# Kernel optimization log

Hardware: AMD Instinct MI355X
Metric: run time of the kernel (lower is better)

The kernel has to match this reference:

```python
import jax, jax.numpy as jnp
import numpy as np

B, D_IN, D_OUT, N_SUBNET, G = 16384, 512, 512, 8, 2


def setup_inputs() -> dict:
    key = jax.random.key(0)
    k_x, k_g, k_w = jax.random.split(key, 3)
    x = jax.random.normal(k_x, (B, D_IN), dtype=jnp.float32)
    groups = jax.random.randint(k_g, (B, G), 0, N_SUBNET, dtype=jnp.int32)
    # per-expert Dense params (the 'subnets')
    W = jax.random.normal(k_w, (N_SUBNET, D_IN, D_OUT), dtype=jnp.float32) * (1.0 / np.sqrt(D_IN))
    b = jnp.zeros((N_SUBNET, D_OUT), dtype=jnp.float32)
    return {"x": x, "groups": groups, "W": W, "b": b}


def reference(x, groups, W, b):
    """SubnetGate: one-hot gated dispatch to per-group subnets + combine.

    Faithful math: gates = one_hot(groups[:, group_col], n_subnet);
    out = sum_e gates[:, e] * subnet_e(x). Since gates are one-hot the
    combine selects exactly one expert output per row (gate weight 1.0).
    """
    group_col = 0
    n_subnet = W.shape[0]
    idx_group = groups[:, group_col]                     # [B]
    gates = jax.nn.one_hot(idx_group, n_subnet, dtype=x.dtype)  # [B, E]
    # run every expert on the full batch (dense reference for the
    # gather-compute-scatter kernel), then gate-combine
    expert_out = jnp.einsum("bi,eio->beo", x, W) + b[None, :, :]  # [B, E, O]
    out = jnp.einsum("be,beo->bo", gates, expert_out)             # [B, O]
    return out
```

## Files before the change

### kernel.cpp

```cpp
#include <hip/hip_runtime.h>
#include <hip/hip_bf16.h>


#define NROWS   16384
#define KDIM    512
#define NDIM    512
#define NEXP    8
#define BM      128
#define BN      128
#define BK      64
#define NT_PER  4
#define KT_PER  8
#define TILE_ELEMS (BN * BK)
#define WS_ROWLIST_OFF 4096
#define WS_WT_OFF      (4096 + NEXP * NROWS * 4)
#define WS_XG_OFF      (WS_WT_OFF + (size_t)NEXP * NT_PER * KT_PER * TILE_ELEMS * 2)
#define WS_NEEDED      (WS_XG_OFF + (size_t)NROWS * KDIM * 2)

typedef __bf16        bf16x8 __attribute__((ext_vector_type(8)));
typedef float         f32x4  __attribute__((ext_vector_type(4)));
typedef unsigned int  u32x4  __attribute__((ext_vector_type(4)));

__device__ __forceinline__ unsigned int f2bf_u(float f) {
    unsigned int u = __builtin_bit_cast(unsigned int, f);
    return (u + 0x7FFFu + ((u >> 16) & 1u)) >> 16;
}

__device__ __forceinline__ void gl_lds16(const void* g, void* l) {
    __builtin_amdgcn_global_load_lds(
        (const __attribute__((address_space(1))) unsigned int*)g,
        (__attribute__((address_space(3))) unsigned int*)l, 16, 0, 0);
}

__device__ __forceinline__ bf16x8 pack_bf8(f32x4 lo, f32x4 hi) {
    u32x4 w;
    w.x = f2bf_u(lo.x) | (f2bf_u(lo.y) << 16);
    w.y = f2bf_u(lo.z) | (f2bf_u(lo.w) << 16);
    w.z = f2bf_u(hi.x) | (f2bf_u(hi.y) << 16);
    w.w = f2bf_u(hi.z) | (f2bf_u(hi.w) << 16);
    return __builtin_bit_cast(bf16x8, w);
}

__global__ void prep_kernel(const float* __restrict__ W,
                            const float* __restrict__ x,
                            const int* __restrict__ groups,
                            int* __restrict__ counts,
                            int* __restrict__ rowlist,
                            unsigned short* __restrict__ Wtile,
                            unsigned short* __restrict__ xg) {
    const int bid = blockIdx.x;
    const int tid = threadIdx.x;

    if (bid < 8) {
        __shared__ int wcnt_s[4];
        __shared__ int woff_s[4];
        __shared__ int runb;
        const int e  = bid;
        const int w  = tid >> 6;
        const int ln = tid & 63;
        const unsigned long long below = (ln == 63) ? ~0ull >> 1
                                                    : (1ull << ln) - 1;
        int* dst = rowlist + e * NROWS;
        if (tid == 0) runb = 0;
        __syncthreads();
        for (int it = 0; it < NROWS / 2048; ++it) {
            int rbase = it * 2048 + tid * 8;
            u32x4 g0 = *(const u32x4*)&groups[rbase * 2];
            u32x4 g1 = *(const u32x4*)&groups[rbase * 2 + 4];
            u32x4 g2 = *(const u32x4*)&groups[rbase * 2 + 8];
            u32x4 g3 = *(const u32x4*)&groups[rbase * 2 + 12];
            bool h[8] = {(int)g0.x == e, (int)g0.z == e,
                         (int)g1.x == e, (int)g1.z == e,
                         (int)g2.x == e, (int)g2.z == e,
                         (int)g3.x == e, (int)g3.z == e};
            unsigned long long m[8];
            int c[8], tot = 0;
            #pragma unroll
            for (int jj = 0; jj < 8; ++jj) {
                m[jj] = __ballot(h[jj]);
                c[jj] = __popcll(m[jj]);
                tot += c[jj];
            }
            if (ln == 0) wcnt_s[w] = tot;
            __syncthreads();
            if (tid == 0) {
                int s = runb;
                #pragma unroll
                for (int i = 0; i < 4; ++i) { woff_s[i] = s; s += wcnt_s[i]; }
                runb = s;
            }
            __syncthreads();
            int base = woff_s[w];
            #pragma unroll
            for (int jj = 0; jj < 8; ++jj) {
                if (h[jj]) dst[base + __popcll(m[jj] & below)] = rbase + jj;
                base += c[jj];
            }
            __syncthreads();
        }
        if (tid == 0) counts[e] = runb;
    } else if (bid < 1032) {
        __shared__ __align__(16) unsigned short tl4[32 * 64];
        const int tb   = bid - 8;
        const int tile = tb >> 2;
        const int qq   = tb & 3;
        const int e  = tile >> 5;
        const int nt = (tile >> 3) & 3;
        const int kt = tile & 7;
        const float* Wb = W + (size_t)e * (KDIM * NDIM);

        const int n   = qq * 32 + (tid & 31);
        const int g   = tid >> 5;
        const int col = nt * BN + n;
        unsigned int p[4];
        #pragma unroll
        for (int jj = 0; jj < 4; ++jj) {
            int k0 = kt * BK + g * 8 + jj * 2;
            unsigned int lo = f2bf_u(Wb[(size_t)k0 * NDIM + col]);
            unsigned int hi = f2bf_u(Wb[(size_t)(k0 + 1) * NDIM + col]);
            p[jj] = lo | (hi << 16);
        }
        *(u32x4*)&tl4[(n & 31) * 64 + (g ^ (n & 7)) * 8] = *(const u32x4*)p;
        __syncthreads();
        unsigned short* dst = Wtile + (size_t)tile * TILE_ELEMS
                                    + ((size_t)qq * 256 + tid) * 8;
        *(u32x4*)dst = *(const u32x4*)&tl4[tid * 8];
    } else {
        const size_t base = ((size_t)(bid - 1032) * 256 + tid) * 16;
        f32x4 v0 = *(const f32x4*)&x[base];
        f32x4 v1 = *(const f32x4*)&x[base + 4];
        f32x4 v2 = *(const f32x4*)&x[base + 8];
        f32x4 v3 = *(const f32x4*)&x[base + 12];
        *(bf16x8*)&xg[base]     = pack_bf8(v0, v1);
        *(bf16x8*)&xg[base + 8] = pack_bf8(v2, v3);
    }
}


#define STAGE_B(KT, BUF)                                                     \
    {                                                                        \
        const unsigned short* _src = wt + (size_t)(KT) * TILE_ELEMS;         \
        _Pragma("unroll")                                                    \
        for (int _i = 0; _i < 4; ++_i) {                                     \
            int _off = (_i * 256 + tid) * 8;                                 \
            gl_lds16(_src + _off, &Bsm[BUF][_off]);                          \
        }                                                                    \
    }

#define LOAD_A_XG(KT, AR)                                                    \
    {                                                                        \
        const unsigned short* _p0 = arow0 + (KT) * BK + q * 8;               \
        const unsigned short* _p1 = arow1 + (KT) * BK + q * 8;               \
        AR[0][0] = *(const bf16x8*)_p0;                                      \
        AR[0][1] = *(const bf16x8*)(_p0 + 32);                               \
        AR[1][0] = *(const bf16x8*)_p1;                                      \
        AR[1][1] = *(const bf16x8*)(_p1 + 32);                               \
    }

#define LOAD_A_F32(KT, AR)                                                   \
    {                                                                        \
        const float* _p0 = afrow0 + (KT) * BK + q * 8;                       \
        const float* _p1 = afrow1 + (KT) * BK + q * 8;                       \
        AR[0][0] = pack_bf8(*(const f32x4*)_p0, *(const f32x4*)(_p0 + 4));   \
        AR[0][1] = pack_bf8(*(const f32x4*)(_p0 + 32),                       \
                            *(const f32x4*)(_p0 + 36));                      \
        AR[1][0] = pack_bf8(*(const f32x4*)_p1, *(const f32x4*)(_p1 + 4));   \
        AR[1][1] = pack_bf8(*(const f32x4*)(_p1 + 32),                       \
                            *(const f32x4*)(_p1 + 36));                      \
    }

#define COMPUTE(BUF, AR)                                                     \
    {                                                                        \
        _Pragma("unroll")                                                    \
        for (int _h = 0; _h < 2; ++_h) {                                     \
            _Pragma("unroll")                                                \
            for (int _ni = 0; _ni < 8; ++_ni) {                              \
                int _n = _ni * 16 + l15;                                     \
                bf16x8 _bf = *(const bf16x8*)&Bsm[BUF][_n * 64 +             \
                             ((_h * 4 + q) ^ (_n & 7)) * 8];                 \
                acc[0][_ni] = __builtin_amdgcn_mfma_f32_16x16x32_bf16(       \
                    AR[0][_h], _bf, acc[0][_ni], 0, 0, 0);                   \
                acc[1][_ni] = __builtin_amdgcn_mfma_f32_16x16x32_bf16(       \
                    AR[1][_h], _bf, acc[1][_ni], 0, 0, 0);                   \
            }                                                                \
        }                                                                    \
    }

#define KSTEP(KT, VM, ACUR, ANXT, LOADA)                                     \
    {                                                                        \
        asm volatile("s_waitcnt vmcnt(" #VM ")" ::: "memory");               \
        __builtin_amdgcn_s_barrier();                                        \
        __builtin_amdgcn_sched_barrier(0);                                   \
        if ((KT) + 2 < KT_PER) LOADA((KT) + 2, ANXT)                         \
        if ((KT) + 3 < KT_PER) STAGE_B((KT) + 3, ((KT) + 3) & 3)             \
        __builtin_amdgcn_s_setprio(1);                                       \
        COMPUTE((KT) & 3, ACUR)                                              \
        __builtin_amdgcn_s_setprio(0);                                       \
    }

#define KLOOP(LOADA)                                                         \
    {                                                                        \
        LOADA(0, aA)                                                         \
        LOADA(1, aB)                                                         \
        KSTEP(0, 16, aA, aC, LOADA)                                          \
        KSTEP(1, 20, aB, aA, LOADA)                                          \
        KSTEP(2, 24, aC, aB, LOADA)                                          \
        KSTEP(3, 16, aA, aC, LOADA)                                          \
        KSTEP(4, 16, aB, aA, LOADA)                                          \
        KSTEP(5, 16, aC, aB, LOADA)                                          \
        KSTEP(6, 12, aA, aC, LOADA)                                          \
        KSTEP(7, 4,  aB, aA, LOADA)                                          \
    }

__global__ __launch_bounds__(256, 2)
void gemm_kernel(const float* __restrict__ x,
                 const unsigned short* __restrict__ xg,
                 const int* __restrict__ counts,
                 const int* __restrict__ rowlist,
                 const unsigned short* __restrict__ Wtile,
                 const float* __restrict__ bias,
                 float* __restrict__ out) {
    __shared__ __align__(16) unsigned short Bsm[4][TILE_ELEMS];

    const int bid = blockIdx.x;
    const int e   = bid & 7;
    const int j   = bid >> 3;
    const int nt  = j & 3;
    const int mt  = j >> 2;
    const int cnt = counts[e];
    const int rb  = mt * BM;
    if (rb >= cnt) return;
    int m_valid = cnt - rb;
    if (m_valid > BM) m_valid = BM;
    const int* rl = rowlist + e * NROWS + rb;

    const int tid = threadIdx.x;
    const int w   = tid >> 6;
    const int ln  = tid & 63;
    const int q   = ln >> 4;
    const int l15 = ln & 15;
    const int wm  = w * 32;

    const int r0i = wm + l15;
    const int r1i = wm + 16 + l15;
    const int ri0 = (r0i < m_valid) ? r0i : 0;
    const int ri1 = (r1i < m_valid) ? r1i : 0;

    const unsigned short* wt =
        Wtile + (size_t)((e * NT_PER + nt) * KT_PER) * TILE_ELEMS;

    f32x4 acc[2][8];
    #pragma unroll
    for (int mi = 0; mi < 2; ++mi)
        #pragma unroll
        for (int ni = 0; ni < 8; ++ni)
            acc[mi][ni] = (f32x4){0.f, 0.f, 0.f, 0.f};

    bf16x8 aA[2][2], aB[2][2], aC[2][2];

    STAGE_B(0, 0)
    STAGE_B(1, 1)
    STAGE_B(2, 2)

    if (xg != nullptr) {
        const unsigned short* arow0 = xg + (size_t)rl[ri0] * KDIM;
        const unsigned short* arow1 = xg + (size_t)rl[ri1] * KDIM;
        KLOOP(LOAD_A_XG)
    } else {
        const float* afrow0 = x + (size_t)rl[ri0] * KDIM;
        const float* afrow1 = x + (size_t)rl[ri1] * KDIM;
        KLOOP(LOAD_A_F32)
    }

    int grow[2][4];
    #pragma unroll
    for (int mi = 0; mi < 2; ++mi)
        #pragma unroll
        for (int r = 0; r < 4; ++r) {
            int mloc = wm + mi * 16 + q * 4 + r;
            grow[mi][r] = (mloc < m_valid) ? rl[mloc] : -1;
        }
    const int ncol0 = nt * BN;
    #pragma unroll
    for (int ni = 0; ni < 8; ++ni) {
        int col = ncol0 + ni * 16 + l15;
        float bv = bias[e * NDIM + col];
        #pragma unroll
        for (int mi = 0; mi < 2; ++mi)
            #pragma unroll
            for (int r = 0; r < 4; ++r)
                if (grow[mi][r] >= 0)
                    __builtin_nontemporal_store(acc[mi][ni][r] + bv,
                        &out[(size_t)grow[mi][r] * NDIM + col]);
    }
}

extern "C" void kernel_launch(void* const* d_in, const int* in_sizes, int n_in,
                              void* d_out, int out_size, void* d_ws, size_t ws_size,
                              hipStream_t stream) {
    const float* x      = (const float*)d_in[0];
    const int*   groups = (const int*)d_in[1];
    const float* W      = (const float*)d_in[2];
    const float* b      = (const float*)d_in[3];
    float*       out    = (float*)d_out;

    char* ws = (char*)d_ws;
    int*            counts  = (int*)ws;
    int*            rowlist = (int*)(ws + WS_ROWLIST_OFF);
    unsigned short* Wtile   = (unsigned short*)(ws + WS_WT_OFF);
    const bool use_xg = (ws_size >= WS_NEEDED);
    unsigned short* xg = use_xg ? (unsigned short*)(ws + WS_XG_OFF) : nullptr;

    prep_kernel<<<use_xg ? 3080 : 1032, 256, 0, stream>>>(
        W, x, groups, counts, rowlist, Wtile, xg);
    gemm_kernel<<<4096, 256, 0, stream>>>(x, xg, counts, rowlist, Wtile, b, out);
}
```

Before: 128.7 us.

## Switch GEMM to full-width 64-row tiles with 512-thread blocks and BK=32

Each block now computes a 64x512 output tile for one expert with 8 waves, instead of 128x128 tiles with 4 waves. Full output width is covered per block, so each gathered A row is loaded once per expert tile rather than once per N-tile. The weight pre-transform now writes 32x512 k-slices without swizzling. B is staged through 128KB of dynamic LDS, which is likely to allow only one block per CU. Each B fragment read from LDS now feeds one MFMA instead of two, and the unswizzled LDS layout may cause bank conflicts.

```diff
diff --git a/kernel.cpp b/kernel.cpp
--- a/kernel.cpp
+++ b/kernel.cpp
@@ -6,15 +6,13 @@
 #define KDIM    512
 #define NDIM    512
 #define NEXP    8
-#define BM      128
-#define BN      128
-#define BK      64
-#define NT_PER  4
-#define KT_PER  8
-#define TILE_ELEMS (BN * BK)
+#define BM      64
+#define BK      32
+#define KT_PER  16
+#define TILE_SH 16384
 #define WS_ROWLIST_OFF 4096
 #define WS_WT_OFF      (4096 + NEXP * NROWS * 4)
-#define WS_XG_OFF      (WS_WT_OFF + (size_t)NEXP * NT_PER * KT_PER * TILE_ELEMS * 2)
+#define WS_XG_OFF      (WS_WT_OFF + (size_t)NEXP * KT_PER * TILE_SH * 2)
 #define WS_NEEDED      (WS_XG_OFF + (size_t)NROWS * KDIM * 2)
 
 typedef __bf16        bf16x8 __attribute__((ext_vector_type(8)));
@@ -99,34 +97,35 @@
             __syncthreads();
         }
         if (tid == 0) counts[e] = runb;
-    } else if (bid < 1032) {
-        __shared__ __align__(16) unsigned short tl4[32 * 64];
-        const int tb   = bid - 8;
-        const int tile = tb >> 2;
-        const int qq   = tb & 3;
-        const int e  = tile >> 5;
-        const int nt = (tile >> 3) & 3;
-        const int kt = tile & 7;
+    } else if (bid < 136) {
+        __shared__ __align__(16) unsigned short tl[TILE_SH];
+        const int t  = bid - 8;
+        const int e  = t >> 4;
+        const int kt = t & 15;
         const float* Wb = W + (size_t)e * (KDIM * NDIM);
-
-        const int n   = qq * 32 + (tid & 31);
-        const int g   = tid >> 5;
-        const int col = nt * BN + n;
-        unsigned int p[4];
         #pragma unroll
-        for (int jj = 0; jj < 4; ++jj) {
-            int k0 = kt * BK + g * 8 + jj * 2;
-            unsigned int lo = f2bf_u(Wb[(size_t)k0 * NDIM + col]);
-            unsigned int hi = f2bf_u(Wb[(size_t)(k0 + 1) * NDIM + col]);
-            p[jj] = lo | (hi << 16);
+        for (int it = 0; it < 8; ++it) {
+            const int n = (it & 1) * 256 + tid;
+            const int g = it >> 1;
+            const int k0 = kt * BK + g * 8;
+            unsigned int p[4];
+            #pragma unroll
+            for (int jj = 0; jj < 4; ++jj) {
+                unsigned int lo = f2bf_u(Wb[(size_t)(k0 + jj * 2) * NDIM + n]);
+                unsigned int hi = f2bf_u(Wb[(size_t)(k0 + jj * 2 + 1) * NDIM + n]);
+                p[jj] = lo | (hi << 16);
+            }
+            *(u32x4*)&tl[n * 32 + g * 8] = *(const u32x4*)p;
         }
-        *(u32x4*)&tl4[(n & 31) * 64 + (g ^ (n & 7)) * 8] = *(const u32x4*)p;
         __syncthreads();
-        unsigned short* dst = Wtile + (size_t)tile * TILE_ELEMS
-                                    + ((size_t)qq * 256 + tid) * 8;
-        *(u32x4*)dst = *(const u32x4*)&tl4[tid * 8];
+        unsigned short* dst = Wtile + (size_t)t * TILE_SH;
+        #pragma unroll
+        for (int it = 0; it < 8; ++it) {
+            int off = (it * 256 + tid) * 8;
+            *(u32x4*)&dst[off] = *(const u32x4*)&tl[off];
+        }
     } else {
-        const size_t base = ((size_t)(bid - 1032) * 256 + tid) * 16;
+        const size_t base = ((size_t)(bid - 136) * 256 + tid) * 16;
         f32x4 v0 = *(const f32x4*)&x[base];
         f32x4 v1 = *(const f32x4*)&x[base + 4];
         f32x4 v2 = *(const f32x4*)&x[base + 8];
@@ -137,52 +136,36 @@
 }
 
 
+extern __shared__ __align__(16) unsigned short Bsm[];
+
 #define STAGE_B(KT, BUF)                                                     \
     {                                                                        \
-        const unsigned short* _src = wt + (size_t)(KT) * TILE_ELEMS;         \
+        const unsigned short* _src = wt + (size_t)(KT) * TILE_SH;            \
         _Pragma("unroll")                                                    \
         for (int _i = 0; _i < 4; ++_i) {                                     \
-            int _off = (_i * 256 + tid) * 8;                                 \
-            gl_lds16(_src + _off, &Bsm[BUF][_off]);                          \
+            int _off = (_i * 512 + tid) * 8;                                 \
+            gl_lds16(_src + _off, &Bsm[(BUF) * TILE_SH + _off]);             \
         }                                                                    \
     }
 
 #define LOAD_A_XG(KT, AR)                                                    \
-    {                                                                        \
-        const unsigned short* _p0 = arow0 + (KT) * BK + q * 8;               \
-        const unsigned short* _p1 = arow1 + (KT) * BK + q * 8;               \
-        AR[0][0] = *(const bf16x8*)_p0;                                      \
-        AR[0][1] = *(const bf16x8*)(_p0 + 32);                               \
-        AR[1][0] = *(const bf16x8*)_p1;                                      \
-        AR[1][1] = *(const bf16x8*)(_p1 + 32);                               \
-    }
+    { AR = *(const bf16x8*)(arow + (KT) * BK + q * 8); }
 
 #define LOAD_A_F32(KT, AR)                                                   \
     {                                                                        \
-        const float* _p0 = afrow0 + (KT) * BK + q * 8;                       \
-        const float* _p1 = afrow1 + (KT) * BK + q * 8;                       \
-        AR[0][0] = pack_bf8(*(const f32x4*)_p0, *(const f32x4*)(_p0 + 4));   \
-        AR[0][1] = pack_bf8(*(const f32x4*)(_p0 + 32),                       \
-                            *(const f32x4*)(_p0 + 36));                      \
-        AR[1][0] = pack_bf8(*(const f32x4*)_p1, *(const f32x4*)(_p1 + 4));   \
-        AR[1][1] = pack_bf8(*(const f32x4*)(_p1 + 32),                       \
-                            *(const f32x4*)(_p1 + 36));                      \
+        const float* _p = afrow + (KT) * BK + q * 8;                         \
+        AR = pack_bf8(*(const f32x4*)_p, *(const f32x4*)(_p + 4));           \
     }
 
 #define COMPUTE(BUF, AR)                                                     \
     {                                                                        \
         _Pragma("unroll")                                                    \
-        for (int _h = 0; _h < 2; ++_h) {                                     \
-            _Pragma("unroll")                                                \
-            for (int _ni = 0; _ni < 8; ++_ni) {                              \
-                int _n = _ni * 16 + l15;                                     \
-                bf16x8 _bf = *(const bf16x8*)&Bsm[BUF][_n * 64 +             \
-                             ((_h * 4 + q) ^ (_n & 7)) * 8];                 \
-                acc[0][_ni] = __builtin_amdgcn_mfma_f32_16x16x32_bf16(       \
-                    AR[0][_h], _bf, acc[0][_ni], 0, 0, 0);                   \
-                acc[1][_ni] = __builtin_amdgcn_mfma_f32_16x16x32_bf16(       \
-                    AR[1][_h], _bf, acc[1][_ni], 0, 0, 0);                   \
-            }                                                                \
+        for (int _ni = 0; _ni < 16; ++_ni) {                                 \
+            int _nn = nh + _ni * 16 + l15;                                   \
+            bf16x8 _bf = *(const bf16x8*)&Bsm[(BUF) * TILE_SH +              \
+                                              _nn * 32 + q * 8];             \
+            acc[_ni] = __builtin_amdgcn_mfma_f32_16x16x32_bf16(              \
+                AR, _bf, acc[_ni], 0, 0, 0);                                 \
         }                                                                    \
     }
 
@@ -202,17 +185,25 @@
     {                                                                        \
         LOADA(0, aA)                                                         \
         LOADA(1, aB)                                                         \
-        KSTEP(0, 16, aA, aC, LOADA)                                          \
-        KSTEP(1, 20, aB, aA, LOADA)                                          \
-        KSTEP(2, 24, aC, aB, LOADA)                                          \
-        KSTEP(3, 16, aA, aC, LOADA)                                          \
-        KSTEP(4, 16, aB, aA, LOADA)                                          \
-        KSTEP(5, 16, aC, aB, LOADA)                                          \
-        KSTEP(6, 12, aA, aC, LOADA)                                          \
-        KSTEP(7, 4,  aB, aA, LOADA)                                          \
-    }
-
-__global__ __launch_bounds__(256, 2)
+        KSTEP(0,  10, aA, aC, LOADA)                                         \
+        KSTEP(1,  11, aB, aA, LOADA)                                         \
+        KSTEP(2,  12, aC, aB, LOADA)                                         \
+        KSTEP(3,  10, aA, aC, LOADA)                                         \
+        KSTEP(4,  10, aB, aA, LOADA)                                         \
+        KSTEP(5,  10, aC, aB, LOADA)                                         \
+        KSTEP(6,  10, aA, aC, LOADA)                                         \
+        KSTEP(7,  10, aB, aA, LOADA)                                         \
+        KSTEP(8,  10, aC, aB, LOADA)                                         \
+        KSTEP(9,  10, aA, aC, LOADA)                                         \
+        KSTEP(10, 10, aB, aA, LOADA)                                         \
+        KSTEP(11, 10, aC, aB, LOADA)                                         \
+        KSTEP(12, 10, aA, aC, LOADA)                                         \
+        KSTEP(13, 10, aB, aA, LOADA)                                         \
+        KSTEP(14, 6,  aC, aB, LOADA)                                         \
+        KSTEP(15, 1,  aA, aC, LOADA)                                         \
+    }
+
+__global__ __launch_bounds__(512, 2)
 void gemm_kernel(const float* __restrict__ x,
                  const unsigned short* __restrict__ xg,
                  const int* __restrict__ counts,
@@ -220,13 +211,9 @@
                  const unsigned short* __restrict__ Wtile,
                  const float* __restrict__ bias,
                  float* __restrict__ out) {
-    __shared__ __align__(16) unsigned short Bsm[4][TILE_ELEMS];
-
     const int bid = blockIdx.x;
     const int e   = bid & 7;
-    const int j   = bid >> 3;
-    const int nt  = j & 3;
-    const int mt  = j >> 2;
+    const int mt  = bid >> 3;
     const int cnt = counts[e];
     const int rb  = mt * BM;
     if (rb >= cnt) return;
@@ -239,59 +226,47 @@
     const int ln  = tid & 63;
     const int q   = ln >> 4;
     const int l15 = ln & 15;
-    const int wm  = w * 32;
-
-    const int r0i = wm + l15;
-    const int r1i = wm + 16 + l15;
-    const int ri0 = (r0i < m_valid) ? r0i : 0;
-    const int ri1 = (r1i < m_valid) ? r1i : 0;
-
-    const unsigned short* wt =
-        Wtile + (size_t)((e * NT_PER + nt) * KT_PER) * TILE_ELEMS;
-
-    f32x4 acc[2][8];
+    const int s   = w >> 1;
+    const int nh  = (w & 1) * 256;
+
+    const int am = s * 16 + l15;
+    const int ri = (am < m_valid) ? am : 0;
+
+    const unsigned short* wt = Wtile + (size_t)e * KT_PER * TILE_SH;
+
+    f32x4 acc[16];
     #pragma unroll
-    for (int mi = 0; mi < 2; ++mi)
-        #pragma unroll
-        for (int ni = 0; ni < 8; ++ni)
-            acc[mi][ni] = (f32x4){0.f, 0.f, 0.f, 0.f};
-
-    bf16x8 aA[2][2], aB[2][2], aC[2][2];
+    for (int ni = 0; ni < 16; ++ni) acc[ni] = (f32x4){0.f, 0.f, 0.f, 0.f};
+
+    bf16x8 aA, aB, aC;
 
     STAGE_B(0, 0)
     STAGE_B(1, 1)
     STAGE_B(2, 2)
 
     if (xg != nullptr) {
-        const unsigned short* arow0 = xg + (size_t)rl[ri0] * KDIM;
-        const unsigned short* arow1 = xg + (size_t)rl[ri1] * KDIM;
+        const unsigned short* arow = xg + (size_t)rl[ri] * KDIM;
         KLOOP(LOAD_A_XG)
     } else {
-        const float* afrow0 = x + (size_t)rl[ri0] * KDIM;
-        const float* afrow1 = x + (size_t)rl[ri1] * KDIM;
+        const float* afrow = x + (size_t)rl[ri] * KDIM;
         KLOOP(LOAD_A_F32)
     }
 
-    int grow[2][4];
+    int grow[4];
     #pragma unroll
-    for (int mi = 0; mi < 2; ++mi)
-        #pragma unroll
-        for (int r = 0; r < 4; ++r) {
-            int mloc = wm + mi * 16 + q * 4 + r;
-            grow[mi][r] = (mloc < m_valid) ? rl[mloc] : -1;
-        }
-    const int ncol0 = nt * BN;
+    for (int r = 0; r < 4; ++r) {
+        int mloc = s * 16 + q * 4 + r;
+        grow[r] = (mloc < m_valid) ? rl[mloc] : -1;
+    }
     #pragma unroll
-    for (int ni = 0; ni < 8; ++ni) {
-        int col = ncol0 + ni * 16 + l15;
+    for (int ni = 0; ni < 16; ++ni) {
+        int col = nh + ni * 16 + l15;
         float bv = bias[e * NDIM + col];
         #pragma unroll
-        for (int mi = 0; mi < 2; ++mi)
-            #pragma unroll
-            for (int r = 0; r < 4; ++r)
-                if (grow[mi][r] >= 0)
-                    __builtin_nontemporal_store(acc[mi][ni][r] + bv,
-                        &out[(size_t)grow[mi][r] * NDIM + col]);
+        for (int r = 0; r < 4; ++r)
+            if (grow[r] >= 0)
+                __builtin_nontemporal_store(acc[ni][r] + bv,
+                    &out[(size_t)grow[r] * NDIM + col]);
     }
 }
 
@@ -311,7 +286,16 @@
     const bool use_xg = (ws_size >= WS_NEEDED);
     unsigned short* xg = use_xg ? (unsigned short*)(ws + WS_XG_OFF) : nullptr;
 
-    prep_kernel<<<use_xg ? 3080 : 1032, 256, 0, stream>>>(
+    static bool attr_set = false;
+    if (!attr_set) {
+        hipFuncSetAttribute((const void*)gemm_kernel,
+                            hipFuncAttributeMaxDynamicSharedMemorySize,
+                            4 * TILE_SH * 2);
+        attr_set = true;
+    }
+
+    prep_kernel<<<use_xg ? 2184 : 136, 256, 0, stream>>>(
         W, x, groups, counts, rowlist, Wtile, xg);
-    gemm_kernel<<<4096, 256, 0, stream>>>(x, xg, counts, rowlist, Wtile, b, out);
-}
+    gemm_kernel<<<2048, 512, 4 * TILE_SH * 2, stream>>>(
+        x, xg, counts, rowlist, Wtile, b, out);
+}
```

Result: slower. 137.0 us (+6.4%).

## Stage whole expert weight slab in LDS once per block with 256-row tiles

Applied to the files above, without the earlier changes.

Each GEMM block now loads the full 512x128 bf16 weight slab for its expert and column strip into dynamic shared memory (128KB) up front, then runs 512 threads over a 256-row tile. It replaces the per-k-step pipelined B staging and barriers with one wait, and uses a fixed grid of 9 row chunks per expert and strip. The intent is to cut redundant weight reloads and barrier overhead. The cost is one block per CU with large LDS use, plus a grid that assumes no expert holds more than 2304 rows. Output stores also change from nontemporal to normal stores.

```diff
diff --git a/kernel.cpp b/kernel.cpp
--- a/kernel.cpp
+++ b/kernel.cpp
@@ -6,12 +6,12 @@
 #define KDIM    512
 #define NDIM    512
 #define NEXP    8
-#define BM      128
+#define BM      256
 #define BN      128
-#define BK      64
 #define NT_PER  4
 #define KT_PER  8
-#define TILE_ELEMS (BN * BK)
+#define MC_PER  9
+#define TILE_ELEMS (BN * 64)
 #define WS_ROWLIST_OFF 4096
 #define WS_WT_OFF      (4096 + NEXP * NROWS * 4)
 #define WS_XG_OFF      (WS_WT_OFF + (size_t)NEXP * NT_PER * KT_PER * TILE_ELEMS * 2)
@@ -115,7 +115,7 @@
         unsigned int p[4];
         #pragma unroll
         for (int jj = 0; jj < 4; ++jj) {
-            int k0 = kt * BK + g * 8 + jj * 2;
+            int k0 = kt * 64 + g * 8 + jj * 2;
             unsigned int lo = f2bf_u(Wb[(size_t)k0 * NDIM + col]);
             unsigned int hi = f2bf_u(Wb[(size_t)(k0 + 1) * NDIM + col]);
             p[jj] = lo | (hi << 16);
@@ -137,82 +137,62 @@
 }
 
 
-#define STAGE_B(KT, BUF)                                                     \
-    {                                                                        \
-        const unsigned short* _src = wt + (size_t)(KT) * TILE_ELEMS;         \
-        _Pragma("unroll")                                                    \
-        for (int _i = 0; _i < 4; ++_i) {                                     \
-            int _off = (_i * 256 + tid) * 8;                                 \
-            gl_lds16(_src + _off, &Bsm[BUF][_off]);                          \
-        }                                                                    \
-    }
-
-#define LOAD_A_XG(KT, AR)                                                    \
-    {                                                                        \
-        const unsigned short* _p0 = arow0 + (KT) * BK + q * 8;               \
-        const unsigned short* _p1 = arow1 + (KT) * BK + q * 8;               \
-        AR[0][0] = *(const bf16x8*)_p0;                                      \
-        AR[0][1] = *(const bf16x8*)(_p0 + 32);                               \
-        AR[1][0] = *(const bf16x8*)_p1;                                      \
-        AR[1][1] = *(const bf16x8*)(_p1 + 32);                               \
-    }
-
-#define LOAD_A_F32(KT, AR)                                                   \
-    {                                                                        \
-        const float* _p0 = afrow0 + (KT) * BK + q * 8;                       \
-        const float* _p1 = afrow1 + (KT) * BK + q * 8;                       \
-        AR[0][0] = pack_bf8(*(const f32x4*)_p0, *(const f32x4*)(_p0 + 4));   \
-        AR[0][1] = pack_bf8(*(const f32x4*)(_p0 + 32),                       \
-                            *(const f32x4*)(_p0 + 36));                      \
-        AR[1][0] = pack_bf8(*(const f32x4*)_p1, *(const f32x4*)(_p1 + 4));   \
-        AR[1][1] = pack_bf8(*(const f32x4*)(_p1 + 32),                       \
-                            *(const f32x4*)(_p1 + 36));                      \
-    }
-
-#define COMPUTE(BUF, AR)                                                     \
+extern __shared__ __align__(16) unsigned short Bsm[];
+
+#define LOAD_A_XG(QT, AR)                                                    \
     {                                                                        \
         _Pragma("unroll")                                                    \
-        for (int _h = 0; _h < 2; ++_h) {                                     \
+        for (int _kh = 0; _kh < 4; ++_kh) {                                  \
+            int _k0 = (QT) * 128 + _kh * 32 + q * 8;                         \
+            AR[0][_kh] = *(const bf16x8*)(arow0 + _k0);                      \
+            AR[1][_kh] = *(const bf16x8*)(arow1 + _k0);                      \
+        }                                                                    \
+    }
+
+#define LOAD_A_F32(QT, AR)                                                   \
+    {                                                                        \
+        _Pragma("unroll")                                                    \
+        for (int _kh = 0; _kh < 4; ++_kh) {                                  \
+            int _k0 = (QT) * 128 + _kh * 32 + q * 8;                         \
+            const float* _p0 = afrow0 + _k0;                                 \
+            const float* _p1 = afrow1 + _k0;                                 \
+            AR[0][_kh] = pack_bf8(*(const f32x4*)_p0, *(const f32x4*)(_p0 + 4)); \
+            AR[1][_kh] = pack_bf8(*(const f32x4*)_p1, *(const f32x4*)(_p1 + 4)); \
+        }                                                                    \
+    }
+
+#define COMPUTE_Q(QT, AR)                                                    \
+    {                                                                        \
+        _Pragma("unroll")                                                    \
+        for (int _kh = 0; _kh < 4; ++_kh) {                                  \
+            const int _t  = (QT) * 4 + _kh;                                  \
+            const int _kt = _t >> 1;                                         \
+            const int _g  = (_t & 1) * 4 + q;                                \
             _Pragma("unroll")                                                \
             for (int _ni = 0; _ni < 8; ++_ni) {                              \
                 int _n = _ni * 16 + l15;                                     \
-                bf16x8 _bf = *(const bf16x8*)&Bsm[BUF][_n * 64 +             \
-                             ((_h * 4 + q) ^ (_n & 7)) * 8];                 \
+                bf16x8 _bf = *(const bf16x8*)&Bsm[_kt * TILE_ELEMS +         \
+                             _n * 64 + (_g ^ (_n & 7)) * 8];                 \
                 acc[0][_ni] = __builtin_amdgcn_mfma_f32_16x16x32_bf16(       \
-                    AR[0][_h], _bf, acc[0][_ni], 0, 0, 0);                   \
+                    AR[0][_kh], _bf, acc[0][_ni], 0, 0, 0);                  \
                 acc[1][_ni] = __builtin_amdgcn_mfma_f32_16x16x32_bf16(       \
-                    AR[1][_h], _bf, acc[1][_ni], 0, 0, 0);                   \
+                    AR[1][_kh], _bf, acc[1][_ni], 0, 0, 0);                  \
             }                                                                \
         }                                                                    \
     }
 
-#define KSTEP(KT, VM, ACUR, ANXT, LOADA)                                     \
-    {                                                                        \
-        asm volatile("s_waitcnt vmcnt(" #VM ")" ::: "memory");               \
-        __builtin_amdgcn_s_barrier();                                        \
-        __builtin_amdgcn_sched_barrier(0);                                   \
-        if ((KT) + 2 < KT_PER) LOADA((KT) + 2, ANXT)                         \
-        if ((KT) + 3 < KT_PER) STAGE_B((KT) + 3, ((KT) + 3) & 3)             \
-        __builtin_amdgcn_s_setprio(1);                                       \
-        COMPUTE((KT) & 3, ACUR)                                              \
-        __builtin_amdgcn_s_setprio(0);                                       \
-    }
-
 #define KLOOP(LOADA)                                                         \
     {                                                                        \
-        LOADA(0, aA)                                                         \
-        LOADA(1, aB)                                                         \
-        KSTEP(0, 16, aA, aC, LOADA)                                          \
-        KSTEP(1, 20, aB, aA, LOADA)                                          \
-        KSTEP(2, 24, aC, aB, LOADA)                                          \
-        KSTEP(3, 16, aA, aC, LOADA)                                          \
-        KSTEP(4, 16, aB, aA, LOADA)                                          \
-        KSTEP(5, 16, aC, aB, LOADA)                                          \
-        KSTEP(6, 12, aA, aC, LOADA)                                          \
-        KSTEP(7, 4,  aB, aA, LOADA)                                          \
-    }
-
-__global__ __launch_bounds__(256, 2)
+        LOADA(1, aR)                                                         \
+        COMPUTE_Q(0, aQ)                                                     \
+        LOADA(2, aQ)                                                         \
+        COMPUTE_Q(1, aR)                                                     \
+        LOADA(3, aR)                                                         \
+        COMPUTE_Q(2, aQ)                                                     \
+        COMPUTE_Q(3, aR)                                                     \
+    }
+
+__global__ __launch_bounds__(512, 1)
 void gemm_kernel(const float* __restrict__ x,
                  const unsigned short* __restrict__ xg,
                  const int* __restrict__ counts,
@@ -220,15 +200,13 @@
                  const unsigned short* __restrict__ Wtile,
                  const float* __restrict__ bias,
                  float* __restrict__ out) {
-    __shared__ __align__(16) unsigned short Bsm[4][TILE_ELEMS];
-
     const int bid = blockIdx.x;
     const int e   = bid & 7;
     const int j   = bid >> 3;
-    const int nt  = j & 3;
-    const int mt  = j >> 2;
+    const int ns  = j & 3;
+    const int mc  = j >> 2;
     const int cnt = counts[e];
-    const int rb  = mt * BM;
+    const int rb  = mc * BM;
     if (rb >= cnt) return;
     int m_valid = cnt - rb;
     if (m_valid > BM) m_valid = BM;
@@ -241,13 +219,19 @@
     const int l15 = ln & 15;
     const int wm  = w * 32;
 
+    const unsigned short* wt =
+        Wtile + (size_t)((e * NT_PER + ns) * KT_PER) * TILE_ELEMS;
+
+    #pragma unroll
+    for (int it = 0; it < 16; ++it) {
+        int off = (it * 512 + tid) * 8;
+        gl_lds16(wt + off, &Bsm[off]);
+    }
+
     const int r0i = wm + l15;
     const int r1i = wm + 16 + l15;
     const int ri0 = (r0i < m_valid) ? r0i : 0;
     const int ri1 = (r1i < m_valid) ? r1i : 0;
-
-    const unsigned short* wt =
-        Wtile + (size_t)((e * NT_PER + nt) * KT_PER) * TILE_ELEMS;
 
     f32x4 acc[2][8];
     #pragma unroll
@@ -256,19 +240,21 @@
         for (int ni = 0; ni < 8; ++ni)
             acc[mi][ni] = (f32x4){0.f, 0.f, 0.f, 0.f};
 
-    bf16x8 aA[2][2], aB[2][2], aC[2][2];
-
-    STAGE_B(0, 0)
-    STAGE_B(1, 1)
-    STAGE_B(2, 2)
+    bf16x8 aQ[2][4], aR[2][4];
 
     if (xg != nullptr) {
         const unsigned short* arow0 = xg + (size_t)rl[ri0] * KDIM;
         const unsigned short* arow1 = xg + (size_t)rl[ri1] * KDIM;
+        LOAD_A_XG(0, aQ)
+        asm volatile("s_waitcnt vmcnt(8)" ::: "memory");
+        __builtin_amdgcn_s_barrier();
         KLOOP(LOAD_A_XG)
     } else {
         const float* afrow0 = x + (size_t)rl[ri0] * KDIM;
         const float* afrow1 = x + (size_t)rl[ri1] * KDIM;
+        LOAD_A_F32(0, aQ)
+        asm volatile("s_waitcnt vmcnt(16)" ::: "memory");
+        __builtin_amdgcn_s_barrier();
         KLOOP(LOAD_A_F32)
     }
 
@@ -280,7 +266,7 @@
             int mloc = wm + mi * 16 + q * 4 + r;
             grow[mi][r] = (mloc < m_valid) ? rl[mloc] : -1;
         }
-    const int ncol0 = nt * BN;
+    const int ncol0 = ns * BN;
     #pragma unroll
     for (int ni = 0; ni < 8; ++ni) {
         int col = ncol0 + ni * 16 + l15;
@@ -290,8 +276,7 @@
             #pragma unroll
             for (int r = 0; r < 4; ++r)
                 if (grow[mi][r] >= 0)
-                    __builtin_nontemporal_store(acc[mi][ni][r] + bv,
-                        &out[(size_t)grow[mi][r] * NDIM + col]);
+                    out[(size_t)grow[mi][r] * NDIM + col] = acc[mi][ni][r] + bv;
     }
 }
 
@@ -311,7 +296,16 @@
     const bool use_xg = (ws_size >= WS_NEEDED);
     unsigned short* xg = use_xg ? (unsigned short*)(ws + WS_XG_OFF) : nullptr;
 
+    static bool attr_set = false;
+    if (!attr_set) {
+        hipFuncSetAttribute((const void*)gemm_kernel,
+                            hipFuncAttributeMaxDynamicSharedMemorySize,
+                            KT_PER * TILE_ELEMS * 2);
+        attr_set = true;
+    }
+
     prep_kernel<<<use_xg ? 3080 : 1032, 256, 0, stream>>>(
         W, x, groups, counts, rowlist, Wtile, xg);
-    gemm_kernel<<<4096, 256, 0, stream>>>(x, xg, counts, rowlist, Wtile, b, out);
-}
+    gemm_kernel<<<NEXP * NT_PER * MC_PER, 512, KT_PER * TILE_ELEMS * 2, stream>>>(
+        x, xg, counts, rowlist, Wtile, b, out);
+}
```

New measurement: 131.1 us. No clear change (+1.9%).

## Drop bf16 staging of x and convert fp32 rows inside the GEMM

Applied to the files above, without the earlier changes.

Removes the prep pass that converted all of x to a bf16 workspace copy. The gathered GEMM now loads fp32 rows directly, with raw loads issued two k-steps ahead and packed to bf16 after each compute step to hide the conversion. The M tile shrinks from 128 to 64 rows with one MFMA row block per wave, and nontemporal output stores become plain stores. The grid is capped at 40 M-tiles per expert, which assumes no expert receives more than 2560 rows; heavier skew would leave rows unwritten. x is also re-read as fp32 once per N tile, which doubles that traffic compared with bf16.

```diff
diff --git a/kernel.cpp b/kernel.cpp
--- a/kernel.cpp
+++ b/kernel.cpp
@@ -6,16 +6,14 @@
 #define KDIM    512
 #define NDIM    512
 #define NEXP    8
-#define BM      128
+#define BM      64
 #define BN      128
-#define BK      64
 #define NT_PER  4
 #define KT_PER  8
-#define TILE_ELEMS (BN * BK)
+#define MT_MAX  40
+#define TILE_ELEMS (BN * 64)
 #define WS_ROWLIST_OFF 4096
 #define WS_WT_OFF      (4096 + NEXP * NROWS * 4)
-#define WS_XG_OFF      (WS_WT_OFF + (size_t)NEXP * NT_PER * KT_PER * TILE_ELEMS * 2)
-#define WS_NEEDED      (WS_XG_OFF + (size_t)NROWS * KDIM * 2)
 
 typedef __bf16        bf16x8 __attribute__((ext_vector_type(8)));
 typedef float         f32x4  __attribute__((ext_vector_type(4)));
@@ -42,12 +40,10 @@
 }
 
 __global__ void prep_kernel(const float* __restrict__ W,
-                            const float* __restrict__ x,
                             const int* __restrict__ groups,
                             int* __restrict__ counts,
                             int* __restrict__ rowlist,
-                            unsigned short* __restrict__ Wtile,
-                            unsigned short* __restrict__ xg) {
+                            unsigned short* __restrict__ Wtile) {
     const int bid = blockIdx.x;
     const int tid = threadIdx.x;
 
@@ -99,7 +95,7 @@
             __syncthreads();
         }
         if (tid == 0) counts[e] = runb;
-    } else if (bid < 1032) {
+    } else {
         __shared__ __align__(16) unsigned short tl4[32 * 64];
         const int tb   = bid - 8;
         const int tile = tb >> 2;
@@ -115,7 +111,7 @@
         unsigned int p[4];
         #pragma unroll
         for (int jj = 0; jj < 4; ++jj) {
-            int k0 = kt * BK + g * 8 + jj * 2;
+            int k0 = kt * 64 + g * 8 + jj * 2;
             unsigned int lo = f2bf_u(Wb[(size_t)k0 * NDIM + col]);
             unsigned int hi = f2bf_u(Wb[(size_t)(k0 + 1) * NDIM + col]);
             p[jj] = lo | (hi << 16);
@@ -125,14 +121,6 @@
         unsigned short* dst = Wtile + (size_t)tile * TILE_ELEMS
                                     + ((size_t)qq * 256 + tid) * 8;
         *(u32x4*)dst = *(const u32x4*)&tl4[tid * 8];
-    } else {
-        const size_t base = ((size_t)(bid - 1032) * 256 + tid) * 16;
-        f32x4 v0 = *(const f32x4*)&x[base];
-        f32x4 v1 = *(const f32x4*)&x[base + 4];
-        f32x4 v2 = *(const f32x4*)&x[base + 8];
-        f32x4 v3 = *(const f32x4*)&x[base + 12];
-        *(bf16x8*)&xg[base]     = pack_bf8(v0, v1);
-        *(bf16x8*)&xg[base + 8] = pack_bf8(v2, v3);
     }
 }
 
@@ -147,74 +135,57 @@
         }                                                                    \
     }
 
-#define LOAD_A_XG(KT, AR)                                                    \
-    {                                                                        \
-        const unsigned short* _p0 = arow0 + (KT) * BK + q * 8;               \
-        const unsigned short* _p1 = arow1 + (KT) * BK + q * 8;               \
-        AR[0][0] = *(const bf16x8*)_p0;                                      \
-        AR[0][1] = *(const bf16x8*)(_p0 + 32);                               \
-        AR[1][0] = *(const bf16x8*)_p1;                                      \
-        AR[1][1] = *(const bf16x8*)(_p1 + 32);                               \
-    }
-
-#define LOAD_A_F32(KT, AR)                                                   \
-    {                                                                        \
-        const float* _p0 = afrow0 + (KT) * BK + q * 8;                       \
-        const float* _p1 = afrow1 + (KT) * BK + q * 8;                       \
-        AR[0][0] = pack_bf8(*(const f32x4*)_p0, *(const f32x4*)(_p0 + 4));   \
-        AR[0][1] = pack_bf8(*(const f32x4*)(_p0 + 32),                       \
-                            *(const f32x4*)(_p0 + 36));                      \
-        AR[1][0] = pack_bf8(*(const f32x4*)_p1, *(const f32x4*)(_p1 + 4));   \
-        AR[1][1] = pack_bf8(*(const f32x4*)(_p1 + 32),                       \
-                            *(const f32x4*)(_p1 + 36));                      \
-    }
-
-#define COMPUTE(BUF, AR)                                                     \
+#define LOAD_RAW(KT, R)                                                      \
+    {                                                                        \
+        const float* _p = afrow + (KT) * 64 + q * 8;                         \
+        R[0] = *(const f32x4*)_p;                                            \
+        R[1] = *(const f32x4*)(_p + 4);                                      \
+        R[2] = *(const f32x4*)(_p + 32);                                     \
+        R[3] = *(const f32x4*)(_p + 36);                                     \
+    }
+
+#define PACK(R, P)                                                           \
+    {                                                                        \
+        P[0] = pack_bf8(R[0], R[1]);                                         \
+        P[1] = pack_bf8(R[2], R[3]);                                         \
+    }
+
+#define COMPUTE(BUF, P)                                                      \
     {                                                                        \
         _Pragma("unroll")                                                    \
-        for (int _h = 0; _h < 2; ++_h) {                                     \
-            _Pragma("unroll")                                                \
-            for (int _ni = 0; _ni < 8; ++_ni) {                              \
-                int _n = _ni * 16 + l15;                                     \
-                bf16x8 _bf = *(const bf16x8*)&Bsm[BUF][_n * 64 +             \
-                             ((_h * 4 + q) ^ (_n & 7)) * 8];                 \
-                acc[0][_ni] = __builtin_amdgcn_mfma_f32_16x16x32_bf16(       \
-                    AR[0][_h], _bf, acc[0][_ni], 0, 0, 0);                   \
-                acc[1][_ni] = __builtin_amdgcn_mfma_f32_16x16x32_bf16(       \
-                    AR[1][_h], _bf, acc[1][_ni], 0, 0, 0);                   \
-            }                                                                \
+        for (int _ni = 0; _ni < 8; ++_ni) {                                  \
+            int _n = _ni * 16 + l15;                                         \
+            bf16x8 _b0 = *(const bf16x8*)&Bsm[BUF][_n * 64 +                 \
+                         (q ^ (_n & 7)) * 8];                                \
+            acc[_ni] = __builtin_amdgcn_mfma_f32_16x16x32_bf16(              \
+                P[0], _b0, acc[_ni], 0, 0, 0);                               \
         }                                                                    \
-    }
-
-#define KSTEP(KT, VM, ACUR, ANXT, LOADA)                                     \
+        _Pragma("unroll")                                                    \
+        for (int _ni = 0; _ni < 8; ++_ni) {                                  \
+            int _n = _ni * 16 + l15;                                         \
+            bf16x8 _b1 = *(const bf16x8*)&Bsm[BUF][_n * 64 +                 \
+                         ((4 + q) ^ (_n & 7)) * 8];                          \
+            acc[_ni] = __builtin_amdgcn_mfma_f32_16x16x32_bf16(              \
+                P[1], _b1, acc[_ni], 0, 0, 0);                               \
+        }                                                                    \
+    }
+
+#define KSTEP(KT, VM, PC, RN, RP, PP)                                        \
     {                                                                        \
         asm volatile("s_waitcnt vmcnt(" #VM ")" ::: "memory");               \
         __builtin_amdgcn_s_barrier();                                        \
         __builtin_amdgcn_sched_barrier(0);                                   \
-        if ((KT) + 2 < KT_PER) LOADA((KT) + 2, ANXT)                         \
+        if ((KT) + 2 < KT_PER) LOAD_RAW((KT) + 2, RN)                        \
         if ((KT) + 3 < KT_PER) STAGE_B((KT) + 3, ((KT) + 3) & 3)             \
         __builtin_amdgcn_s_setprio(1);                                       \
-        COMPUTE((KT) & 3, ACUR)                                              \
+        COMPUTE((KT) & 3, PC)                                                \
         __builtin_amdgcn_s_setprio(0);                                       \
-    }
-
-#define KLOOP(LOADA)                                                         \
-    {                                                                        \
-        LOADA(0, aA)                                                         \
-        LOADA(1, aB)                                                         \
-        KSTEP(0, 16, aA, aC, LOADA)                                          \
-        KSTEP(1, 20, aB, aA, LOADA)                                          \
-        KSTEP(2, 24, aC, aB, LOADA)                                          \
-        KSTEP(3, 16, aA, aC, LOADA)                                          \
-        KSTEP(4, 16, aB, aA, LOADA)                                          \
-        KSTEP(5, 16, aC, aB, LOADA)                                          \
-        KSTEP(6, 12, aA, aC, LOADA)                                          \
-        KSTEP(7, 4,  aB, aA, LOADA)                                          \
+        __builtin_amdgcn_sched_barrier(0);                                   \
+        if ((KT) + 1 < KT_PER) PACK(RP, PP)                                  \
     }
 
 __global__ __launch_bounds__(256, 2)
 void gemm_kernel(const float* __restrict__ x,
-                 const unsigned short* __restrict__ xg,
                  const int* __restrict__ counts,
                  const int* __restrict__ rowlist,
                  const unsigned short* __restrict__ Wtile,
@@ -224,9 +195,8 @@
 
     const int bid = blockIdx.x;
     const int e   = bid & 7;
-    const int j   = bid >> 3;
-    const int nt  = j & 3;
-    const int mt  = j >> 2;
+    const int nt  = (bid >> 3) & 3;
+    const int mt  = bid >> 5;
     const int cnt = counts[e];
     const int rb  = mt * BM;
     if (rb >= cnt) return;
@@ -239,59 +209,53 @@
     const int ln  = tid & 63;
     const int q   = ln >> 4;
     const int l15 = ln & 15;
-    const int wm  = w * 32;
-
-    const int r0i = wm + l15;
-    const int r1i = wm + 16 + l15;
-    const int ri0 = (r0i < m_valid) ? r0i : 0;
-    const int ri1 = (r1i < m_valid) ? r1i : 0;
+    const int wm  = w * 16;
+
+    const int am = wm + l15;
+    const int ri = (am < m_valid) ? am : 0;
+    const float* afrow = x + (size_t)rl[ri] * KDIM;
 
     const unsigned short* wt =
         Wtile + (size_t)((e * NT_PER + nt) * KT_PER) * TILE_ELEMS;
 
-    f32x4 acc[2][8];
+    f32x4 acc[8];
     #pragma unroll
-    for (int mi = 0; mi < 2; ++mi)
-        #pragma unroll
-        for (int ni = 0; ni < 8; ++ni)
-            acc[mi][ni] = (f32x4){0.f, 0.f, 0.f, 0.f};
-
-    bf16x8 aA[2][2], aB[2][2], aC[2][2];
+    for (int ni = 0; ni < 8; ++ni) acc[ni] = (f32x4){0.f, 0.f, 0.f, 0.f};
+
+    f32x4  rA[4], rB[4];
+    bf16x8 pA[2], pB[2];
 
     STAGE_B(0, 0)
+    LOAD_RAW(0, rA)
     STAGE_B(1, 1)
+    LOAD_RAW(1, rB)
     STAGE_B(2, 2)
-
-    if (xg != nullptr) {
-        const unsigned short* arow0 = xg + (size_t)rl[ri0] * KDIM;
-        const unsigned short* arow1 = xg + (size_t)rl[ri1] * KDIM;
-        KLOOP(LOAD_A_XG)
-    } else {
-        const float* afrow0 = x + (size_t)rl[ri0] * KDIM;
-        const float* afrow1 = x + (size_t)rl[ri1] * KDIM;
-        KLOOP(LOAD_A_F32)
-    }
-
-    int grow[2][4];
+    PACK(rA, pA)
+
+    KSTEP(0, 12, pA, rA, rB, pB)
+    KSTEP(1, 16, pB, rB, rA, pA)
+    KSTEP(2, 16, pA, rA, rB, pB)
+    KSTEP(3, 16, pB, rB, rA, pA)
+    KSTEP(4, 16, pA, rA, rB, pB)
+    KSTEP(5, 16, pB, rB, rA, pA)
+    KSTEP(6, 12, pA, rA, rB, pB)
+    KSTEP(7, 4,  pB, rB, rA, pA)
+
+    int grow[4];
     #pragma unroll
-    for (int mi = 0; mi < 2; ++mi)
-        #pragma unroll
-        for (int r = 0; r < 4; ++r) {
-            int mloc = wm + mi * 16 + q * 4 + r;
-            grow[mi][r] = (mloc < m_valid) ? rl[mloc] : -1;
-        }
+    for (int r = 0; r < 4; ++r) {
+        int mloc = wm + q * 4 + r;
+        grow[r] = (mloc < m_valid) ? rl[mloc] : -1;
+    }
     const int ncol0 = nt * BN;
     #pragma unroll
     for (int ni = 0; ni < 8; ++ni) {
         int col = ncol0 + ni * 16 + l15;
         float bv = bias[e * NDIM + col];
         #pragma unroll
-        for (int mi = 0; mi < 2; ++mi)
-            #pragma unroll
-            for (int r = 0; r < 4; ++r)
-                if (grow[mi][r] >= 0)
-                    __builtin_nontemporal_store(acc[mi][ni][r] + bv,
-                        &out[(size_t)grow[mi][r] * NDIM + col]);
+        for (int r = 0; r < 4; ++r)
+            if (grow[r] >= 0)
+                out[(size_t)grow[r] * NDIM + col] = acc[ni][r] + bv;
     }
 }
 
@@ -308,10 +272,8 @@
     int*            counts  = (int*)ws;
     int*            rowlist = (int*)(ws + WS_ROWLIST_OFF);
     unsigned short* Wtile   = (unsigned short*)(ws + WS_WT_OFF);
-    const bool use_xg = (ws_size >= WS_NEEDED);
-    unsigned short* xg = use_xg ? (unsigned short*)(ws + WS_XG_OFF) : nullptr;
-
-    prep_kernel<<<use_xg ? 3080 : 1032, 256, 0, stream>>>(
-        W, x, groups, counts, rowlist, Wtile, xg);
-    gemm_kernel<<<4096, 256, 0, stream>>>(x, xg, counts, rowlist, Wtile, b, out);
-}
+
+    prep_kernel<<<1032, 256, 0, stream>>>(W, groups, counts, rowlist, Wtile);
+    gemm_kernel<<<NEXP * NT_PER * MT_MAX, 256, 0, stream>>>(
+        x, counts, rowlist, Wtile, b, out);
+}
```

Result: no change. 131.0 us (+1.8%).
